# Kernel tuning notes

Measured on AMD Instinct MI355X. Metric: run time of the kernel, lower is better.

The kernel has to match this reference:

```python
import jax, jax.numpy as jnp
import numpy as np

B, N, M, F, D = 4, 8, 64, 128, 128
EPS = 1e-5


def setup_inputs() -> dict:
    key = jax.random.key(0)
    ks = jax.random.split(key, 6)
    s1 = 1.0 / np.sqrt(5 * F)
    s2 = 1.0 / np.sqrt(F)
    return {
        "x": jax.random.normal(ks[0], (B, N, M, F), dtype=jnp.float32),
        "W1": jax.random.uniform(ks[1], (F, 5 * F), jnp.float32, -s1, s1),
        "b1": jax.random.uniform(ks[2], (F,), jnp.float32, -s1, s1),
        "gamma": jnp.ones((F,), jnp.float32),
        "beta": jnp.zeros((F,), jnp.float32),
        "bias_p": jax.random.normal(ks[3], (F,), jnp.float32) * 0.02,
        "W2": jax.random.uniform(ks[4], (D, F), jnp.float32, -s2, s2),
        "b2": jax.random.uniform(ks[5], (D,), jnp.float32, -s2, s2),
    }


def reference(x, W1, b1, gamma, beta, bias_p, W2, b2):
    b, n, m, f = x.shape
    e = jnp.eye(m, dtype=x.dtype)[:, :, None]        # (M,M,1) diagonal mask
    xi = x[:, :, :, None, :]                          # value indexed by row i
    xj = x[:, :, None, :, :]                          # value indexed by col j
    mean = jnp.mean(x, axis=2, keepdims=True)[:, :, :, None, :]  # (B,N,1,1,F)
    shp = (b, n, m, m, f)
    # Equivariant 1->2 lift: [diag(x), row-bcast, col-bcast, diag(mean), mean-bcast]
    xAll = jnp.concatenate([
        xi * e,
        jnp.broadcast_to(xi, shp),
        jnp.broadcast_to(xj, shp),
        jnp.broadcast_to(mean * e, shp),
        jnp.broadcast_to(mean, shp),
    ], axis=-1)                                       # (B,N,M,M,5F)
    h = jnp.einsum('bnijk,fk->bnijf', xAll, W1) + b1  # fc1
    mu = jnp.mean(h, axis=-1, keepdims=True)
    var = jnp.mean((h - mu) ** 2, axis=-1, keepdims=True)
    h = (h - mu) / jnp.sqrt(var + EPS) * gamma + beta # LayerNorm
    h = jax.nn.relu(h)
    h = h + bias_p * e                                # diagonal-masked bias
    return jnp.einsum('bnijf,df->bnijd', h, W2) + b2  # fc2 -> (B,N,M,M,D)
```

## Files before the change

kernel.cpp:

```cpp
#include <hip/hip_runtime.h>

typedef __bf16 bf16x4 __attribute__((ext_vector_type(4)));
typedef __bf16 bf16x8 __attribute__((ext_vector_type(8)));
typedef float  f32x4v __attribute__((ext_vector_type(4)));

#define HS 136


__global__ __launch_bounds__(256) void k1_prep(
    const float* __restrict__ x, const float* __restrict__ W1,
    const float* __restrict__ b1, const float* __restrict__ W2,
    float* __restrict__ Up, float* __restrict__ V, float* __restrict__ Dg,
    __bf16* __restrict__ W2b)
{
  __shared__ float Xs[64][132];
  __shared__ float meanv[128], mwd[128], mwe[128];

  const int tid = threadIdx.x;
  const int bn  = blockIdx.x >> 3;
  const int g   = blockIdx.x & 7;

  const float4* xv = reinterpret_cast<const float4*>(x + (size_t)bn * 8192);
#pragma unroll
  for (int it = 0; it < 8; ++it) {
    int p = tid + 256 * it;
    int r = p >> 5, c4 = p & 31;
    *reinterpret_cast<float4*>(&Xs[r][4 * c4]) = xv[p];
  }

  if (g == 0) {
    const float4* w2v = reinterpret_cast<const float4*>(W2);
#pragma unroll
    for (int it = 0; it < 16; ++it) {
      int p = tid + 256 * it;
      float4 v = w2v[p];
      bf16x4 hv;
      hv[0] = (__bf16)v.x; hv[1] = (__bf16)v.y;
      hv[2] = (__bf16)v.z; hv[3] = (__bf16)v.w;
      reinterpret_cast<bf16x4*>(W2b)[p] = hv;
    }
  }
  __syncthreads();

  if (tid < 128) {
    float s = 0.f;
    for (int r = 0; r < 64; ++r) s += Xs[r][tid];
    meanv[tid] = s * (1.f / 64.f);
  }
  __syncthreads();

  if (tid < 128) {
    const float* wd = W1 + (size_t)tid * 640 + 384;
    const float* we = W1 + (size_t)tid * 640 + 512;
    float ad = 0.f, ae = 0.f;
    for (int k = 0; k < 128; ++k) {
      float mk = meanv[k];
      ad += mk * wd[k];
      ae += mk * we[k];
    }
    mwd[tid] = ad;
    mwe[tid] = ae + b1[tid];
  }
  __syncthreads();

  for (int dd = tid; dd < 384; dd += 256) {
    int part = dd >> 7;
    int f    = dd & 127;
    const float4* wrow =
        reinterpret_cast<const float4*>(W1 + (size_t)f * 640 + part * 128);
    float acc[8] = {};
    for (int kc = 0; kc < 32; ++kc) {
      float4 wv = wrow[kc];
#pragma unroll
      for (int r = 0; r < 8; ++r) {
        float4 xr = *reinterpret_cast<const float4*>(&Xs[8 * g + r][4 * kc]);
        acc[r] += xr.x * wv.x + xr.y * wv.y + xr.z * wv.z + xr.w * wv.w;
      }
    }
    float  add = (part == 0) ? mwd[f] : (part == 1 ? mwe[f] : 0.f);
    float* op  = (part == 0) ? Dg : (part == 1 ? Up : V);
#pragma unroll
    for (int r = 0; r < 8; ++r)
      op[((size_t)bn * 64 + 8 * g + r) * 128 + f] = acc[r] + add;
  }
}

__global__ __launch_bounds__(256) void k2_main(
    const float* __restrict__ Up, const float* __restrict__ V,
    const float* __restrict__ Dg, const __bf16* __restrict__ W2b,
    const float* __restrict__ gamma, const float* __restrict__ beta,
    const float* __restrict__ bias_p, const float* __restrict__ b2,
    float* __restrict__ out)
{
  __shared__ __align__(16) __bf16 W2s[128 * HS];
  __shared__ __align__(16) __bf16 Hs[64 * HS];

  const int tid  = threadIdx.x;
  const int bid  = blockIdx.x;
  const int bn   = bid >> 6;
  const int i    = bid & 63;
  const int lane = tid & 63;
  const int w    = tid >> 6;

  {
    const uint4* w2v = reinterpret_cast<const uint4*>(W2b);
#pragma unroll
    for (int it = 0; it < 8; ++it) {
      int p   = tid + 256 * it;
      int row = p >> 4;
      int col = (p & 15) * 8;
      *reinterpret_cast<uint4*>(&W2s[row * HS + col]) = w2v[p];
    }
  }

  {
    const int c    = lane & 31;
    const int half = lane >> 5;
    const size_t base = (size_t)bn * 64;
    const float4 up4 = reinterpret_cast<const float4*>(Up + (base + i) * 128)[c];
    const float4 dg4 = reinterpret_cast<const float4*>(Dg + (base + i) * 128)[c];
    const float4 g4  = reinterpret_cast<const float4*>(gamma)[c];
    const float4 be4 = reinterpret_cast<const float4*>(beta)[c];
    const float4 bp4 = reinterpret_cast<const float4*>(bias_p)[c];
#pragma unroll
    for (int it = 0; it < 8; ++it) {
      int r = 8 * it + 2 * w + half;
      float4 v4 = reinterpret_cast<const float4*>(V + (base + r) * 128)[c];
      float h0 = v4.x + up4.x, h1 = v4.y + up4.y;
      float h2 = v4.z + up4.z, h3 = v4.w + up4.w;
      if (r == i) { h0 += dg4.x; h1 += dg4.y; h2 += dg4.z; h3 += dg4.w; }
      float s = h0 + h1 + h2 + h3;
      float q = h0 * h0 + h1 * h1 + h2 * h2 + h3 * h3;
#pragma unroll
      for (int off = 16; off > 0; off >>= 1) {
        s += __shfl_xor(s, off, 32);
        q += __shfl_xor(q, off, 32);
      }
      float mu   = s * (1.f / 128.f);
      float var  = q * (1.f / 128.f) - mu * mu;
      float rstd = rsqrtf(var + 1e-5f);
      h0 = fmaxf(fmaf((h0 - mu) * rstd, g4.x, be4.x), 0.f);
      h1 = fmaxf(fmaf((h1 - mu) * rstd, g4.y, be4.y), 0.f);
      h2 = fmaxf(fmaf((h2 - mu) * rstd, g4.z, be4.z), 0.f);
      h3 = fmaxf(fmaf((h3 - mu) * rstd, g4.w, be4.w), 0.f);
      if (r == i) { h0 += bp4.x; h1 += bp4.y; h2 += bp4.z; h3 += bp4.w; }
      bf16x4 hv;
      hv[0] = (__bf16)h0; hv[1] = (__bf16)h1;
      hv[2] = (__bf16)h2; hv[3] = (__bf16)h3;
      *reinterpret_cast<bf16x4*>(&Hs[r * HS + 4 * c]) = hv;
    }
  }
  __syncthreads();

  const int m    = lane & 15;
  const int quad = lane >> 4;
  bf16x8 af[4];
#pragma unroll
  for (int ks = 0; ks < 4; ++ks)
    af[ks] = *reinterpret_cast<const bf16x8*>(
        &Hs[(16 * w + m) * HS + 32 * ks + 8 * quad]);

  const size_t obase = (size_t)bid * 8192;
#pragma unroll
  for (int t = 0; t < 8; ++t) {
    f32x4v a = {0.f, 0.f, 0.f, 0.f};
#pragma unroll
    for (int ks = 0; ks < 4; ++ks) {
      bf16x8 bf = *reinterpret_cast<const bf16x8*>(
          &W2s[(16 * t + m) * HS + 32 * ks + 8 * quad]);
      a = __builtin_amdgcn_mfma_f32_16x16x32_bf16(af[ks], bf, a, 0, 0, 0);
    }
    const int d = 16 * t + m;
    const float b2v = b2[d];
#pragma unroll
    for (int rg = 0; rg < 4; ++rg) {
      int j = 16 * w + 4 * quad + rg;
      out[obase + (size_t)j * 128 + d] = a[rg] + b2v;
    }
  }
}

extern "C" void kernel_launch(void* const* d_in, const int* in_sizes, int n_in,
                              void* d_out, int out_size, void* d_ws, size_t ws_size,
                              hipStream_t stream) {
  const float* x      = (const float*)d_in[0];
  const float* W1     = (const float*)d_in[1];
  const float* b1     = (const float*)d_in[2];
  const float* gamma  = (const float*)d_in[3];
  const float* beta   = (const float*)d_in[4];
  const float* bias_p = (const float*)d_in[5];
  const float* W2     = (const float*)d_in[6];
  const float* b2     = (const float*)d_in[7];

  float*  Up  = (float*)d_ws;
  float*  V   = Up + 2048 * 128;
  float*  Dg  = V + 2048 * 128;
  __bf16* W2b = (__bf16*)(Dg + 2048 * 128);

  k1_prep<<<256, 256, 0, stream>>>(x, W1, b1, W2, Up, V, Dg, W2b);
  k2_main<<<2048, 256, 0, stream>>>(Up, V, Dg, W2b, gamma, beta, bias_p, b2,
                                    (float*)d_out);
}
```

Before: 121.0 us.

## Compute prep projections with split-bf16 MFMA and batch V loads in main kernel

The prep kernel now computes the three per-row projections of x against W1 on matrix cores. It splits fp32 operands into hi/lo bf16 pairs and uses three MFMAs per step to keep near-fp32 accuracy, replacing the scalar FMA loops. Work is re-split into 6 blocks per (b,n) across 192 blocks, and the mean is accumulated through shared-memory atomics during the load. The main kernel also issues all eight V row loads before the LayerNorm loop to increase memory-level parallelism. The cost is extra conversion work and redundant x staging in every block.

```diff
diff --git a/kernel.cpp b/kernel.cpp
--- a/kernel.cpp
+++ b/kernel.cpp
@@ -13,22 +13,45 @@
     float* __restrict__ Up, float* __restrict__ V, float* __restrict__ Dg,
     __bf16* __restrict__ W2b)
 {
-  __shared__ float Xs[64][132];
-  __shared__ float meanv[128], mwd[128], mwe[128];
-
-  const int tid = threadIdx.x;
-  const int bn  = blockIdx.x >> 3;
-  const int g   = blockIdx.x & 7;
-
-  const float4* xv = reinterpret_cast<const float4*>(x + (size_t)bn * 8192);
-#pragma unroll
-  for (int it = 0; it < 8; ++it) {
-    int p = tid + 256 * it;
-    int r = p >> 5, c4 = p & 31;
-    *reinterpret_cast<float4*>(&Xs[r][4 * c4]) = xv[p];
-  }
-
-  if (g == 0) {
+  __shared__ __align__(16) __bf16 Xhi[64 * HS];
+  __shared__ __align__(16) __bf16 Xlo[64 * HS];
+  __shared__ float msum[128], pm[256], mw[128];
+
+  const int tid  = threadIdx.x;
+  const int bn   = blockIdx.x / 6;
+  const int ch   = blockIdx.x % 6;
+  const int lane = tid & 63;
+  const int w    = tid >> 6;
+  const int pidx = ch >> 1;
+
+  if (tid < 128) msum[tid] = 0.f;
+  __syncthreads();
+
+  {
+    const float4* xv = reinterpret_cast<const float4*>(x + (size_t)bn * 8192);
+    const int c = tid & 31;
+    float4 ps = {0.f, 0.f, 0.f, 0.f};
+#pragma unroll
+    for (int it = 0; it < 8; ++it) {
+      int p = tid + 256 * it;
+      int r = p >> 5;
+      float4 v = xv[p];
+      ps.x += v.x; ps.y += v.y; ps.z += v.z; ps.w += v.w;
+      bf16x4 hv, lv;
+      hv[0] = (__bf16)v.x; lv[0] = (__bf16)(v.x - (float)hv[0]);
+      hv[1] = (__bf16)v.y; lv[1] = (__bf16)(v.y - (float)hv[1]);
+      hv[2] = (__bf16)v.z; lv[2] = (__bf16)(v.z - (float)hv[2]);
+      hv[3] = (__bf16)v.w; lv[3] = (__bf16)(v.w - (float)hv[3]);
+      *reinterpret_cast<bf16x4*>(&Xhi[r * HS + 4 * c]) = hv;
+      *reinterpret_cast<bf16x4*>(&Xlo[r * HS + 4 * c]) = lv;
+    }
+    atomicAdd(&msum[4 * c + 0], ps.x);
+    atomicAdd(&msum[4 * c + 1], ps.y);
+    atomicAdd(&msum[4 * c + 2], ps.z);
+    atomicAdd(&msum[4 * c + 3], ps.w);
+  }
+
+  if (ch == 4) {
     const float4* w2v = reinterpret_cast<const float4*>(W2);
 #pragma unroll
     for (int it = 0; it < 16; ++it) {
@@ -42,46 +65,67 @@
   }
   __syncthreads();
 
-  if (tid < 128) {
-    float s = 0.f;
-    for (int r = 0; r < 64; ++r) s += Xs[r][tid];
-    meanv[tid] = s * (1.f / 64.f);
-  }
-  __syncthreads();
-
-  if (tid < 128) {
-    const float* wd = W1 + (size_t)tid * 640 + 384;
-    const float* we = W1 + (size_t)tid * 640 + 512;
-    float ad = 0.f, ae = 0.f;
-    for (int k = 0; k < 128; ++k) {
-      float mk = meanv[k];
-      ad += mk * wd[k];
-      ae += mk * we[k];
-    }
-    mwd[tid] = ad;
-    mwe[tid] = ae + b1[tid];
-  }
-  __syncthreads();
-
-  for (int dd = tid; dd < 384; dd += 256) {
-    int part = dd >> 7;
-    int f    = dd & 127;
-    const float4* wrow =
-        reinterpret_cast<const float4*>(W1 + (size_t)f * 640 + part * 128);
-    float acc[8] = {};
-    for (int kc = 0; kc < 32; ++kc) {
-      float4 wv = wrow[kc];
-#pragma unroll
-      for (int r = 0; r < 8; ++r) {
-        float4 xr = *reinterpret_cast<const float4*>(&Xs[8 * g + r][4 * kc]);
-        acc[r] += xr.x * wv.x + xr.y * wv.y + xr.z * wv.z + xr.w * wv.w;
+  {
+    const int f  = tid & 127;
+    const int hh = tid >> 7;
+    float acc = 0.f;
+    if (pidx < 2) {
+      const float4* wv4 = reinterpret_cast<const float4*>(
+          W1 + (size_t)f * 640 + (pidx == 0 ? 384 : 512) + hh * 64);
+#pragma unroll
+      for (int kc = 0; kc < 16; ++kc) {
+        float4 wv = wv4[kc];
+        int k = hh * 64 + 4 * kc;
+        acc += msum[k] * wv.x + msum[k + 1] * wv.y +
+               msum[k + 2] * wv.z + msum[k + 3] * wv.w;
       }
     }
-    float  add = (part == 0) ? mwd[f] : (part == 1 ? mwe[f] : 0.f);
-    float* op  = (part == 0) ? Dg : (part == 1 ? Up : V);
-#pragma unroll
-    for (int r = 0; r < 8; ++r)
-      op[((size_t)bn * 64 + 8 * g + r) * 128 + f] = acc[r] + add;
+    pm[tid] = acc;
+  }
+  __syncthreads();
+  if (tid < 128)
+    mw[tid] = (pm[tid] + pm[tid + 128]) * (1.f / 64.f) +
+              (pidx == 1 ? b1[tid] : 0.f);
+  __syncthreads();
+
+  const int m    = lane & 15;
+  const int quad = lane >> 4;
+  bf16x8 ahi[4], alo[4];
+#pragma unroll
+  for (int ks = 0; ks < 4; ++ks) {
+    ahi[ks] = *reinterpret_cast<const bf16x8*>(&Xhi[(16 * w + m) * HS + 32 * ks + 8 * quad]);
+    alo[ks] = *reinterpret_cast<const bf16x8*>(&Xlo[(16 * w + m) * HS + 32 * ks + 8 * quad]);
+  }
+
+  float* rout = (pidx == 0) ? Dg : (pidx == 1 ? Up : V);
+#pragma unroll
+  for (int tt = 0; tt < 4; ++tt) {
+    const int fout = (((4 * ch + tt) & 7) * 16) + m;
+    const float* wrow = W1 + (size_t)fout * 640 + pidx * 128;
+    f32x4v a = {0.f, 0.f, 0.f, 0.f};
+#pragma unroll
+    for (int ks = 0; ks < 4; ++ks) {
+      float4 w0 = *reinterpret_cast<const float4*>(wrow + 32 * ks + 8 * quad);
+      float4 w1 = *reinterpret_cast<const float4*>(wrow + 32 * ks + 8 * quad + 4);
+      bf16x8 bhi, blo;
+      bhi[0] = (__bf16)w0.x; blo[0] = (__bf16)(w0.x - (float)bhi[0]);
+      bhi[1] = (__bf16)w0.y; blo[1] = (__bf16)(w0.y - (float)bhi[1]);
+      bhi[2] = (__bf16)w0.z; blo[2] = (__bf16)(w0.z - (float)bhi[2]);
+      bhi[3] = (__bf16)w0.w; blo[3] = (__bf16)(w0.w - (float)bhi[3]);
+      bhi[4] = (__bf16)w1.x; blo[4] = (__bf16)(w1.x - (float)bhi[4]);
+      bhi[5] = (__bf16)w1.y; blo[5] = (__bf16)(w1.y - (float)bhi[5]);
+      bhi[6] = (__bf16)w1.z; blo[6] = (__bf16)(w1.z - (float)bhi[6]);
+      bhi[7] = (__bf16)w1.w; blo[7] = (__bf16)(w1.w - (float)bhi[7]);
+      a = __builtin_amdgcn_mfma_f32_16x16x32_bf16(ahi[ks], bhi, a, 0, 0, 0);
+      a = __builtin_amdgcn_mfma_f32_16x16x32_bf16(alo[ks], bhi, a, 0, 0, 0);
+      a = __builtin_amdgcn_mfma_f32_16x16x32_bf16(ahi[ks], blo, a, 0, 0, 0);
+    }
+    const float addv = mw[fout];
+#pragma unroll
+    for (int rg = 0; rg < 4; ++rg) {
+      int ii = 16 * w + 4 * quad + rg;
+      rout[((size_t)bn * 64 + ii) * 128 + fout] = a[rg] + addv;
+    }
   }
 }
 
@@ -122,10 +166,16 @@
     const float4 g4  = reinterpret_cast<const float4*>(gamma)[c];
     const float4 be4 = reinterpret_cast<const float4*>(beta)[c];
     const float4 bp4 = reinterpret_cast<const float4*>(bias_p)[c];
+    float4 v4s[8];
 #pragma unroll
     for (int it = 0; it < 8; ++it) {
       int r = 8 * it + 2 * w + half;
-      float4 v4 = reinterpret_cast<const float4*>(V + (base + r) * 128)[c];
+      v4s[it] = reinterpret_cast<const float4*>(V + (base + r) * 128)[c];
+    }
+#pragma unroll
+    for (int it = 0; it < 8; ++it) {
+      int r = 8 * it + 2 * w + half;
+      float4 v4 = v4s[it];
       float h0 = v4.x + up4.x, h1 = v4.y + up4.y;
       float h2 = v4.z + up4.z, h3 = v4.w + up4.w;
       if (r == i) { h0 += dg4.x; h1 += dg4.y; h2 += dg4.z; h3 += dg4.w; }
@@ -197,7 +247,7 @@
   float*  Dg  = V + 2048 * 128;
   __bf16* W2b = (__bf16*)(Dg + 2048 * 128);
 
-  k1_prep<<<256, 256, 0, stream>>>(x, W1, b1, W2, Up, V, Dg, W2b);
+  k1_prep<<<192, 256, 0, stream>>>(x, W1, b1, W2, Up, V, Dg, W2b);
   k2_main<<<2048, 256, 0, stream>>>(Up, V, Dg, W2b, gamma, beta, bias_p, b2,
                                     (float*)d_out);
 }
```

New measurement: 111.6 us. -7.7%, faster.
